# Optimization experiments

Hardware: AMD Instinct MI355X
Metric: run time of the kernel (lower is better)

## Reference

```python
import jax, jax.numpy as jnp
import numpy as np

B, C, T, H, W = 2, 128, 4, 32, 32
L = 6  # number_of_layers


def setup_inputs() -> dict:
    key = jax.random.key(0)
    ks = jax.random.split(key, 7)
    scale = 0.05  # keep pre-softmax logits in a sane range
    return {
        "x": jax.random.normal(ks[0], (B, C, T, H, W), dtype=jnp.float32),
        "W1": jax.random.normal(ks[1], (L, C, C), dtype=jnp.float32) * scale,
        "b1": jax.random.normal(ks[2], (L, C), dtype=jnp.float32) * scale,
        "W2": jax.random.normal(ks[3], (L, C, C), dtype=jnp.float32) * scale,
        "b2": jax.random.normal(ks[4], (L, C), dtype=jnp.float32) * scale,
        "Wg": jax.random.normal(ks[5], (L, C, C), dtype=jnp.float32) * scale,
        "bg": jax.random.normal(ks[6], (L, C), dtype=jnp.float32) * scale,
    }


def reference(x, W1, b1, W2, b2, Wg, bg):
    b, c, t, h, w = x.shape
    n = t * h * w  # THW tokens
    xf = x.reshape(b, c, n)  # [B, C, N], token order = (t, h, w) flattened
    inv_sqrt = 1.0 / jnp.sqrt(jnp.asarray(n, x.dtype))
    num_layers = W1.shape[0]
    acc = jnp.zeros((b, n, c), dtype=x.dtype)
    for l in range(num_layers):
        # conv3d 1x1x1 == per-token channel matmul + bias
        f1 = jnp.einsum('oc,bcn->bno', W1[l], xf) + b1[l]            # queries [B, N, C]
        f2 = jnp.einsum('oc,bcn->bon', W2[l], xf) + b2[l][:, None]   # keys    [B, C, N]
        scores = jnp.einsum('bnc,bcm->bnm', f1, f2) * inv_sqrt       # [B, N, N]
        # NOTE: original uses nn.Softmax(dim=1) -> normalize over the ROW (query) axis
        attn = jax.nn.softmax(scores, axis=1)
        g1 = jnp.einsum('oc,bcn->bno', Wg[l], xf) + bg[l]            # values [B, N, C]
        acc = acc + jnp.einsum('bnm,bmc->bnc', attn, g1)
    out = acc / num_layers                                           # mean over heads
    out = out.transpose(0, 2, 1).reshape(b, c, t, h, w)
    return out + x                                                    # residual
```

## Files before the change

kernel.cpp:

```cpp
#include <hip/hip_runtime.h>
#include <hip/hip_bf16.h>

#define BCNT 2
#define CCH  128
#define NTOK 4096
#define NLAY 6
#define QK8SCALE 0.15014030f

using f32x4   = __attribute__((ext_vector_type(4))) float;
using f32x16  = __attribute__((ext_vector_type(16))) float;
using bf16x8  = __attribute__((ext_vector_type(8))) short;

static __device__ __forceinline__ ushort f2bf(float f) {
  unsigned u = __float_as_uint(f);
  u += 0x7FFF + ((u >> 16) & 1);
  return (ushort)(u >> 16);
}
static __device__ __forceinline__ uint pk2(float lo, float hi) {
  uint r;
  asm volatile("v_cvt_pk_bf16_f32 %0, %1, %2" : "=v"(r) : "v"(lo), "v"(hi));
  return r;
}
static __device__ __forceinline__ uint pkf8(float a, float b) {
  uint r = 0;
  asm volatile("v_cvt_pk_fp8_f32 %0, %1, %2" : "+v"(r) : "v"(a), "v"(b));
  return r;
}
static __device__ __forceinline__ void plswap(uint& a, uint& b) {
  asm volatile("v_permlane32_swap_b32 %0, %1" : "+v"(a), "+v"(b));
}
static __device__ __forceinline__ float vexp2(float x) {
  float r;
  asm("v_exp_f32 %0, %1" : "=v"(r) : "v"(x));
  return r;
}
static __device__ __forceinline__ void dma16(const void* g, void* l) {
  __builtin_amdgcn_global_load_lds(
      (const __attribute__((address_space(1))) unsigned int*)g,
      (__attribute__((address_space(3))) unsigned int*)l, 16, 0, 0);
}

__global__ __launch_bounds__(256) void transpose_kernel(
    const float* __restrict__ x, ushort* __restrict__ xT)
{
  __shared__ ushort ls[64][68];
  const int t = threadIdx.x;
  const int ntile = blockIdx.x * 64, ctile = blockIdx.y * 64, b = blockIdx.z;
  const float* xb = x + ((size_t)b * CCH + ctile) * NTOK + ntile;
  #pragma unroll
  for (int p = 0; p < 4; ++p) {
    int idx = p * 256 + t;
    int cc = idx >> 4, n4 = (idx & 15) * 4;
    float4 v = *(const float4*)(xb + (size_t)cc * NTOK + n4);
    ls[cc][n4 + 0] = f2bf(v.x); ls[cc][n4 + 1] = f2bf(v.y);
    ls[cc][n4 + 2] = f2bf(v.z); ls[cc][n4 + 3] = f2bf(v.w);
  }
  __syncthreads();
  ushort* ob = xT + ((size_t)b * NTOK + ntile) * CCH + ctile;
  #pragma unroll
  for (int p = 0; p < 16; ++p) {
    int idx = p * 256 + t;
    int nn = idx >> 6, cc = idx & 63;
    ob[(size_t)nn * CCH + cc] = ls[cc][nn];
  }
}

__global__ __launch_bounds__(256) void wcvt_kernel(
    const float* __restrict__ W1, const float* __restrict__ W2,
    const float* __restrict__ Wg, ushort* __restrict__ Wb)
{
  const float* src = (blockIdx.y == 0) ? W1 : (blockIdx.y == 1) ? W2 : Wg;
  const size_t base = (size_t)blockIdx.y * NLAY * CCH * CCH;
  const size_t i = (size_t)blockIdx.x * 1024 + threadIdx.x * 4;
  float4 w = *(const float4*)(src + i);
  uint2 o = make_uint2(pk2(w.x, w.y), pk2(w.z, w.w));
  *(uint2*)(Wb + base + i) = o;
}

__global__ __launch_bounds__(256) void qkv_kernel(
    const ushort* __restrict__ xT, const ushort* __restrict__ Wb,
    const float* __restrict__ b1, const float* __restrict__ b2,
    const float* __restrict__ bg,
    uchar* __restrict__ q8, uchar* __restrict__ k8, ushort* __restrict__ vv,
    int l0)
{
  __shared__ __align__(16) ushort as[128][128];
  __shared__ __align__(16) ushort bs[128][128];
  const int t = threadIdx.x;
  const int lane = t & 63, wave = t >> 6;
  const int ntile = blockIdx.x * 128;
  const int which = blockIdx.y;
  const int z = blockIdx.z;
  const int b = z & 1, lidx = z >> 1, layer = l0 + lidx;
  const float* bias = (which == 0 ? b1 : which == 1 ? b2 : bg)
                      + (size_t)layer * CCH;
  const ushort* W = Wb + ((size_t)which * NLAY + layer) * CCH * CCH;
  const ushort* xb = xT + ((size_t)b * NTOK + ntile) * CCH;
  const ushort* ga = (which < 2) ? xb : W;
  const ushort* gb = (which < 2) ? W : xb;

  #pragma unroll
  for (int j = 0; j < 8; ++j) {
    int row = wave * 32 + j * 4 + (lane >> 4);
    int qs = (lane & 15) ^ (row & 15);
    dma16(ga + (size_t)row * 128 + qs * 8, &as[wave * 32 + j * 4][0]);
    dma16(gb + (size_t)row * 128 + qs * 8, &bs[wave * 32 + j * 4][0]);
  }
  asm volatile("s_waitcnt vmcnt(0)" ::: "memory");
  __syncthreads();

  const int l16 = lane & 15, lg = lane >> 4;
  const int wr = (wave >> 1) * 64, wc = (wave & 1) * 64;

  f32x4 acc[4][4];
  #pragma unroll
  for (int i = 0; i < 4; ++i)
    #pragma unroll
    for (int j = 0; j < 4; ++j) acc[i][j] = (f32x4)0.f;

  #pragma unroll
  for (int kk = 0; kk < 4; ++kk) {
    bf16x8 a[4], bb[4];
    #pragma unroll
    for (int i = 0; i < 4; ++i) {
      int row = wr + i * 16 + l16;
      a[i] = *(const bf16x8*)&as[row][(((kk * 4 + lg) ^ (row & 15)) * 8)];
    }
    #pragma unroll
    for (int j = 0; j < 4; ++j) {
      int row = wc + j * 16 + l16;
      bb[j] = *(const bf16x8*)&bs[row][(((kk * 4 + lg) ^ (row & 15)) * 8)];
    }
    #pragma unroll
    for (int i = 0; i < 4; ++i)
      #pragma unroll
      for (int j = 0; j < 4; ++j)
        acc[i][j] = __builtin_amdgcn_mfma_f32_16x16x32_bf16(a[i], bb[j], acc[i][j], 0, 0, 0);
  }

  if (which < 2) {
    uchar* o8 = (which == 0 ? q8 : k8) + (size_t)z * NTOK * CCH;
    #pragma unroll
    for (int j = 0; j < 4; ++j) {
      float bv = bias[wc + j * 16 + l16];
      #pragma unroll
      for (int i = 0; i < 4; ++i)
        #pragma unroll
        for (int r = 0; r < 4; ++r) {
          int n = ntile + wr + i * 16 + lg * 4 + r;
          float val = (acc[i][j][r] + bv) * QK8SCALE;
          uint pb = pkf8(val, val);
          o8[(size_t)n * CCH + wc + j * 16 + l16] = (uchar)pb;
        }
    }
  } else {
    ushort* oz = vv + (size_t)z * NTOK * CCH;
    #pragma unroll
    for (int i = 0; i < 4; ++i)
      #pragma unroll
      for (int r = 0; r < 4; ++r) {
        int o = wr + i * 16 + lg * 4 + r;
        float bv = bias[o];
        #pragma unroll
        for (int j = 0; j < 4; ++j)
          oz[(size_t)o * NTOK + ntile + wc + j * 16 + l16] = f2bf(acc[i][j][r] + bv);
      }
  }
}

__global__ __launch_bounds__(256, 3) void dsum_kernel(
    const uchar* __restrict__ q8, const uchar* __restrict__ k8,
    float* __restrict__ D)
{
  __shared__ __align__(16) uchar ks[3][32][256];
  const int t = threadIdx.x;
  const int lane = t & 63, wave = t >> 6;
  const int l31 = lane & 31, hi = lane >> 5;

  const int bid = blockIdx.x, ngrid = gridDim.x;
  const int wg = (bid & 7) * (ngrid >> 3) + (bid >> 3);
  const int z = wg >> 6, rem = wg & 63;
  const int nbase = (rem >> 3) * 512 + wave * 128;
  const int mstart = (rem & 7) * 512;

  const uchar* qz = q8 + (size_t)z * NTOK * CCH;
  const uchar* kz = k8 + (size_t)z * NTOK * CCH;

  long qf[4][8];
  #pragma unroll
  for (int nb = 0; nb < 4; ++nb)
    #pragma unroll
    for (int ck = 0; ck < 8; ++ck)
      qf[nb][ck] = *(const long*)(qz + (size_t)(nbase + nb * 32 + l31) * CCH
                                  + ck * 16 + hi * 8);

#define STAGEK(p, msub) do {                                                  \
    _Pragma("unroll")                                                         \
    for (int d_ = 0; d_ < 2; ++d_) {                                          \
      int R_ = wave * 8 + d_ * 4 + (lane >> 4);                               \
      int qs_ = (lane & 15) ^ (R_ & 15);                                      \
      dma16(kz + (size_t)((msub) + 2 * R_ + (qs_ >> 3)) * CCH + (qs_ & 7) * 16, \
            &ks[p][wave * 8 + d_ * 4][0]);                                    \
    }                                                                         \
  } while (0)

  STAGEK(0, mstart);
  STAGEK(1, mstart + 64);
  asm volatile("s_waitcnt vmcnt(2)" ::: "memory");
  __builtin_amdgcn_s_barrier();

  float* Dz = D + (size_t)z * NTOK;
  #pragma unroll
  for (int st = 0; st < 8; ++st) {
    if (st + 2 < 8) STAGEK((st + 2) % 3, mstart + (st + 2) * 64);
    const int cur = st % 3;

    #pragma unroll
    for (int mbi = 0; mbi < 2; ++mbi) {
      const int mb = mbi ^ (wave & 1);
      f32x16 ss[4];
      #pragma unroll
      for (int nb = 0; nb < 4; ++nb) ss[nb] = (f32x16)0.f;
      const int row = mb * 32 + l31;
      const int R = row >> 1;
      __builtin_amdgcn_s_setprio(1);
      #pragma unroll
      for (int ck = 0; ck < 8; ++ck) {
        int qs = ((row & 1) << 3) | ck;
        long kf = *(const long*)&ks[cur][R][((qs ^ (R & 15)) << 4) + hi * 8];
        #pragma unroll
        for (int nb = 0; nb < 4; ++nb)
          ss[nb] = __builtin_amdgcn_mfma_f32_32x32x16_fp8_fp8(qf[nb][ck], kf, ss[nb], 0, 0, 0);
      }
      __builtin_amdgcn_s_setprio(0);
      float s = 0.f;
      #pragma unroll
      for (int nb = 0; nb < 4; ++nb)
        #pragma unroll
        for (int r = 0; r < 16; ++r) s += vexp2(ss[nb][r]);
      s += __shfl_xor(s, 32);
      if (lane < 32)
        atomicAdd(&Dz[mstart + st * 64 + mb * 32 + l31], s);
    }
    if (st < 7) {
      asm volatile("s_waitcnt vmcnt(4)" ::: "memory");
      __builtin_amdgcn_s_barrier();
    }
  }
#undef STAGEK
}

__global__ __launch_bounds__(256) void scalev_kernel(
    ushort* __restrict__ vv, const float* __restrict__ D)
{
  size_t i8 = ((size_t)blockIdx.x * 256 + threadIdx.x) * 8;
  int m = (int)(i8 & (NTOK - 1));
  int z = (int)(i8 >> 19);
  const float* dp = D + (size_t)z * NTOK + m;
  uint4 u = *(uint4*)(vv + i8);
  float4 d0 = *(const float4*)dp;
  float4 d1 = *(const float4*)(dp + 4);
  uint w[4] = {u.x, u.y, u.z, u.w};
  float ds[8] = {d0.x, d0.y, d0.z, d0.w, d1.x, d1.y, d1.z, d1.w};
  #pragma unroll
  for (int d = 0; d < 4; ++d) {
    float r0 = __builtin_amdgcn_rcpf(ds[2 * d] * (float)NLAY);
    float r1 = __builtin_amdgcn_rcpf(ds[2 * d + 1] * (float)NLAY);
    float lo = __uint_as_float(w[d] << 16) * r0;
    float hi = __uint_as_float(w[d] & 0xFFFF0000u) * r1;
    w[d] = pk2(lo, hi);
  }
  *(uint4*)(vv + i8) = make_uint4(w[0], w[1], w[2], w[3]);
}

template <int NL, bool PART>
__global__ __launch_bounds__(256, 2) void pv_kernel(
    const uchar* __restrict__ q8, const uchar* __restrict__ k8,
    const ushort* __restrict__ vv, float* __restrict__ accG,
    ushort* __restrict__ part)
{
  __shared__ __align__(16) uchar  ks[3][32][256];
  __shared__ __align__(16) ushort vs[3][64][128];
  const int t = threadIdx.x;
  const int lane = t & 63, wave = t >> 6;
  const int l31 = lane & 31, hi = lane >> 5;
  const size_t PLZ = (size_t)NTOK * CCH;

  const int bid = blockIdx.x, ngrid = gridDim.x;
  const int wg = (bid & 7) * (ngrid >> 3) + (bid >> 3);
  const int b = wg >> 8, rem = wg & 255;
  const int ng = rem & 15, ms = rem >> 4;
  const int nbase = ng * 256 + wave * 64;
  const int mstart = ms * 256;

  long qf[2][8];
  f32x16 oacc[2][4];
  #pragma unroll
  for (int nb = 0; nb < 2; ++nb)
    #pragma unroll
    for (int cb = 0; cb < 4; ++cb) oacc[nb][cb] = (f32x16)0.f;

#define LOADQ(lidx) do {                                                      \
    const uchar* qz_ = q8 + (size_t)((lidx) * 2 + b) * PLZ;                   \
    _Pragma("unroll")                                                         \
    for (int nb_ = 0; nb_ < 2; ++nb_)                                         \
      _Pragma("unroll")                                                       \
      for (int ck_ = 0; ck_ < 8; ++ck_)                                       \
        qf[nb_][ck_] = *(const long*)(qz_ + (size_t)(nbase + nb_ * 32 + l31) * CCH \
                                      + ck_ * 16 + hi * 8);                   \
  } while (0)

#define STAGE(p, tau) do {                                                    \
    const uchar*  kz_ = k8 + (size_t)(((tau) >> 2) * 2 + b) * PLZ;            \
    const ushort* vz_ = vv + (size_t)(((tau) >> 2) * 2 + b) * PLZ;            \
    const int msub_ = mstart + ((tau) & 3) * 64;                              \
    _Pragma("unroll")                                                         \
    for (int d_ = 0; d_ < 2; ++d_) {                                          \
      int R_ = wave * 8 + d_ * 4 + (lane >> 4);                               \
      int qs_ = (lane & 15) ^ (R_ & 15);                                      \
      dma16(kz_ + (size_t)(msub_ + 2 * R_ + (qs_ >> 3)) * CCH + (qs_ & 7) * 16, \
            &ks[p][wave * 8 + d_ * 4][0]);                                    \
    }                                                                         \
    _Pragma("unroll")                                                         \
    for (int d_ = 0; d_ < 4; ++d_) {                                          \
      int r_ = wave * 16 + d_ * 4 + (lane >> 4);                              \
      int qs_ = (lane & 15) ^ (r_ & 15);                                      \
      dma16(vz_ + (size_t)(r_ + 64 * (qs_ >> 3)) * NTOK + msub_ + (qs_ & 7) * 8, \
            &vs[p][wave * 16 + d_ * 4][0]);                                   \
    }                                                                         \
  } while (0)

  STAGE(0, 0);
  STAGE(1, 1);

  #pragma unroll 3
  for (int tau = 0; tau < 4 * NL; ++tau) {
    asm volatile("s_waitcnt vmcnt(6)" ::: "memory");
    __builtin_amdgcn_s_barrier();
    if ((tau & 3) == 0) LOADQ(tau >> 2);
    if (tau + 2 < 4 * NL) STAGE((tau + 2) % 3, tau + 2);
    const int cur = tau % 3;

    #pragma unroll
    for (int mbi = 0; mbi < 2; ++mbi) {
      const int mb = mbi ^ (wave & 1);
      f32x16 ss[2];
      ss[0] = (f32x16)0.f; ss[1] = (f32x16)0.f;
      const int row = mb * 32 + l31;
      const int R = row >> 1;
      __builtin_amdgcn_s_setprio(1);
      #pragma unroll
      for (int ck = 0; ck < 8; ++ck) {
        int qs = ((row & 1) << 3) | ck;
        long kf = *(const long*)&ks[cur][R][((qs ^ (R & 15)) << 4) + hi * 8];
        ss[0] = __builtin_amdgcn_mfma_f32_32x32x16_fp8_fp8(kf, qf[0][ck], ss[0], 0, 0, 0);
        ss[1] = __builtin_amdgcn_mfma_f32_32x32x16_fp8_fp8(kf, qf[1][ck], ss[1], 0, 0, 0);
      }
      __builtin_amdgcn_s_setprio(0);

      bf16x8 paL[2][2];
      #pragma unroll
      for (int nb = 0; nb < 2; ++nb) {
        #pragma unroll
        for (int s = 0; s < 2; ++s) {
          uint w0 = pk2(vexp2(ss[nb][8 * s + 0]), vexp2(ss[nb][8 * s + 1]));
          uint w1 = pk2(vexp2(ss[nb][8 * s + 2]), vexp2(ss[nb][8 * s + 3]));
          uint w2 = pk2(vexp2(ss[nb][8 * s + 4]), vexp2(ss[nb][8 * s + 5]));
          uint w3 = pk2(vexp2(ss[nb][8 * s + 6]), vexp2(ss[nb][8 * s + 7]));
          plswap(w0, w2);
          plswap(w1, w3);
          uint4 ui = make_uint4(w0, w1, w2, w3);
          paL[nb][s] = *(bf16x8*)&ui;
        }
      }

      __builtin_amdgcn_s_setprio(1);
      #pragma unroll
      for (int cb = 0; cb < 4; ++cb) {
        const int c = cb * 32 + l31;
        const int r = c & 63;
        #pragma unroll
        for (int s = 0; s < 2; ++s) {
          int qs = ((c >> 6) << 3) | (4 * mb + 2 * s + hi);
          bf16x8 vf = *(const bf16x8*)&vs[cur][r][(qs ^ (r & 15)) * 8];
          oacc[0][cb] = __builtin_amdgcn_mfma_f32_32x32x16_bf16(paL[0][s], vf, oacc[0][cb], 0, 0, 0);
          oacc[1][cb] = __builtin_amdgcn_mfma_f32_32x32x16_bf16(paL[1][s], vf, oacc[1][cb], 0, 0, 0);
        }
      }
      __builtin_amdgcn_s_setprio(0);
    }
  }
#undef STAGE
#undef LOADQ

  if (PART) {
    ushort* pz = part + (size_t)(ms * BCNT + b) * NTOK * CCH;
    #pragma unroll
    for (int nb = 0; nb < 2; ++nb)
      #pragma unroll
      for (int cb = 0; cb < 4; ++cb)
        #pragma unroll
        for (int r = 0; r < 16; ++r) {
          int n = nbase + nb * 32 + (r & 3) + 8 * (r >> 2) + 4 * hi;
          pz[(size_t)n * CCH + cb * 32 + l31] = f2bf(oacc[nb][cb][r]);
        }
  } else {
    float* az = accG + (size_t)b * NTOK * CCH;
    #pragma unroll
    for (int nb = 0; nb < 2; ++nb)
      #pragma unroll
      for (int cb = 0; cb < 4; ++cb)
        #pragma unroll
        for (int r = 0; r < 16; ++r) {
          int n = nbase + nb * 32 + (r & 3) + 8 * (r >> 2) + 4 * hi;
          atomicAdd(&az[(size_t)n * CCH + cb * 32 + l31], oacc[nb][cb][r]);
        }
  }
}

__global__ __launch_bounds__(256) void finalize_kernel(
    const float* __restrict__ acc, const float* __restrict__ x,
    float* __restrict__ out)
{
  __shared__ float ts[64][65];
  const int t = threadIdx.x;
  const int ntile = blockIdx.x * 64, ctile = blockIdx.y * 64, b = blockIdx.z;
  const float* ab = acc + ((size_t)b * NTOK + ntile) * CCH + ctile;
  #pragma unroll
  for (int p = 0; p < 4; ++p) {
    int idx = p * 256 + t;
    int nn = idx >> 4, c4 = (idx & 15) * 4;
    float4 v = *(const float4*)(ab + (size_t)nn * CCH + c4);
    ts[nn][c4 + 0] = v.x; ts[nn][c4 + 1] = v.y;
    ts[nn][c4 + 2] = v.z; ts[nn][c4 + 3] = v.w;
  }
  __syncthreads();
  const size_t base = ((size_t)b * CCH + ctile) * NTOK + ntile;
  #pragma unroll
  for (int p = 0; p < 16; ++p) {
    int idx = p * 256 + t;
    int nn = idx & 63, cc = idx >> 6;
    size_t o = base + (size_t)cc * NTOK + nn;
    out[o] = ts[nn][cc] + x[o];
  }
}

__global__ __launch_bounds__(256) void finalize_part_kernel(
    const ushort* __restrict__ part, const float* __restrict__ x,
    float* __restrict__ out)
{
  __shared__ float ts[64][65];
  const int t = threadIdx.x;
  const int ntile = blockIdx.x * 64, ctile = blockIdx.y * 64, b = blockIdx.z;
  #pragma unroll
  for (int p = 0; p < 4; ++p) {
    int idx = p * 256 + t;
    int nn = idx >> 4, c4 = (idx & 15) * 4;
    float s0 = 0.f, s1 = 0.f, s2 = 0.f, s3 = 0.f;
    const ushort* pp = part + ((size_t)b * NTOK + ntile + nn) * CCH + ctile + c4;
    #pragma unroll
    for (int msi = 0; msi < 16; ++msi) {
      uint2 u = *(const uint2*)(pp + (size_t)msi * BCNT * NTOK * CCH);
      s0 += __uint_as_float(u.x << 16);
      s1 += __uint_as_float(u.x & 0xFFFF0000u);
      s2 += __uint_as_float(u.y << 16);
      s3 += __uint_as_float(u.y & 0xFFFF0000u);
    }
    ts[nn][c4 + 0] = s0; ts[nn][c4 + 1] = s1;
    ts[nn][c4 + 2] = s2; ts[nn][c4 + 3] = s3;
  }
  __syncthreads();
  const size_t base = ((size_t)b * CCH + ctile) * NTOK + ntile;
  #pragma unroll
  for (int p = 0; p < 16; ++p) {
    int idx = p * 256 + t;
    int nn = idx & 63, cc = idx >> 6;
    size_t o = base + (size_t)cc * NTOK + nn;
    out[o] = ts[nn][cc] + x[o];
  }
}

extern "C" void kernel_launch(void* const* d_in, const int* in_sizes, int n_in,
                              void* d_out, int out_size, void* d_ws, size_t ws_size,
                              hipStream_t stream)
{
  const float* x  = (const float*)d_in[0];
  const float* W1 = (const float*)d_in[1];
  const float* b1 = (const float*)d_in[2];
  const float* W2 = (const float*)d_in[3];
  const float* b2 = (const float*)d_in[4];
  const float* Wg = (const float*)d_in[5];
  const float* bg = (const float*)d_in[6];
  float* out = (float*)d_out;

  const size_t PL = (size_t)BCNT * NTOK * CCH;
  const size_t DSZ = (size_t)BCNT * NTOK;
  const size_t WBSZ = (size_t)3 * NLAY * CCH * CCH;

  int nb = 1;
  for (int cand : {6, 3, 2}) {
    size_t need = PL * 2 + (size_t)cand * (PL * 2 + PL + PL) + WBSZ * 2
                + (size_t)cand * DSZ * 4 + PL * 4;
    if (ws_size >= need) { nb = cand; break; }
  }
  size_t need_base = PL * 2 + (size_t)nb * (PL * 2 + PL + PL) + WBSZ * 2
                   + (size_t)nb * DSZ * 4 + PL * 4;
  bool usePart = (nb == 6) && (ws_size >= need_base + 16 * PL * 2);

  char* p = (char*)d_ws;
  ushort* xT = (ushort*)p; p += PL * 2;
  ushort* vv = (ushort*)p; p += (size_t)nb * PL * 2;
  uchar*  q8 = (uchar*)p;  p += (size_t)nb * PL;
  uchar*  k8 = (uchar*)p;  p += (size_t)nb * PL;
  ushort* Wb = (ushort*)p; p += WBSZ * 2;
  float*  D  = (float*)p;  p += (size_t)nb * DSZ * 4;
  float*  acc= (float*)p;  p += PL * 4;
  ushort* part = (ushort*)p;

  if (!usePart) hipMemsetAsync(acc, 0, PL * 4, stream);
  transpose_kernel<<<dim3(NTOK / 64, CCH / 64, BCNT), 256, 0, stream>>>(x, xT);
  wcvt_kernel<<<dim3(96, 3), 256, 0, stream>>>(W1, W2, Wg, Wb);

  for (int l0 = 0; l0 < NLAY; l0 += nb) {
    const int LB = nb * BCNT;
    hipMemsetAsync(D, 0, (size_t)LB * NTOK * 4, stream);
    qkv_kernel<<<dim3(NTOK / 128, 3, LB), 256, 0, stream>>>(
        xT, Wb, b1, b2, bg, q8, k8, vv, l0);
    dsum_kernel<<<dim3(LB * 64), 256, 0, stream>>>(q8, k8, D);
    scalev_kernel<<<dim3(LB * 256), 256, 0, stream>>>(vv, D);
    const dim3 pvg(BCNT * 256);
    if (usePart) {
      pv_kernel<6, true><<<pvg, 256, 0, stream>>>(q8, k8, vv, acc, part);
    } else {
      switch (nb) {
        case 6: pv_kernel<6, false><<<pvg, 256, 0, stream>>>(q8, k8, vv, acc, part); break;
        case 3: pv_kernel<3, false><<<pvg, 256, 0, stream>>>(q8, k8, vv, acc, part); break;
        case 2: pv_kernel<2, false><<<pvg, 256, 0, stream>>>(q8, k8, vv, acc, part); break;
        default: pv_kernel<1, false><<<pvg, 256, 0, stream>>>(q8, k8, vv, acc, part); break;
      }
    }
  }
  if (usePart)
    finalize_part_kernel<<<dim3(NTOK / 64, CCH / 64, BCNT), 256, 0, stream>>>(part, x, out);
  else
    finalize_kernel<<<dim3(NTOK / 64, CCH / 64, BCNT), 256, 0, stream>>>(acc, x, out);
}
```

Measured before the change: 168.4 us.

## Use FP8 PV matmul and 32x32x64 scaled MFMA for QK and PV

Switches the QK score matmuls in dsum and pv kernels from 32x32x16 fp8 MFMA to the wider 32x32x64 f8f6f4 scaled MFMA, loading 32-byte fragments. Converts the normalized V to fp8, with a pre-scale of 4096 to keep values in fp8 range, and the softmax probabilities to fp8, so the PV product also runs on fp8 MFMA; the output is descaled at accumulation. This halves the V bytes staged through LDS and the MFMA count, at the cost of lower precision in P and V and an extra fp8 V buffer in the workspace.

Result: slower. 235.0 us (+39.5%).

```diff
diff --git a/kernel.cpp b/kernel.cpp
--- a/kernel.cpp
+++ b/kernel.cpp
@@ -6,10 +6,12 @@
 #define NTOK 4096
 #define NLAY 6
 #define QK8SCALE 0.15014030f
+#define VDESC 2.44140625e-4f
 
 using f32x4   = __attribute__((ext_vector_type(4))) float;
 using f32x16  = __attribute__((ext_vector_type(16))) float;
 using bf16x8  = __attribute__((ext_vector_type(8))) short;
+using i32x8   = __attribute__((ext_vector_type(8))) int;
 
 static __device__ __forceinline__ ushort f2bf(float f) {
   unsigned u = __float_as_uint(f);
@@ -21,6 +23,12 @@
   asm volatile("v_cvt_pk_bf16_f32 %0, %1, %2" : "=v"(r) : "v"(lo), "v"(hi));
   return r;
 }
+static __device__ __forceinline__ uint pkf8x4(float a, float b, float c, float d) {
+  uint r;
+  asm volatile("v_cvt_pk_fp8_f32 %0, %1, %2" : "=v"(r) : "v"(a), "v"(b));
+  asm volatile("v_cvt_pk_fp8_f32 %0, %1, %2 op_sel:[0,0,1]" : "+v"(r) : "v"(c), "v"(d));
+  return r;
+}
 static __device__ __forceinline__ uint pkf8(float a, float b) {
   uint r = 0;
   asm volatile("v_cvt_pk_fp8_f32 %0, %1, %2" : "+v"(r) : "v"(a), "v"(b));
@@ -38,6 +46,15 @@
   __builtin_amdgcn_global_load_lds(
       (const __attribute__((address_space(1))) unsigned int*)g,
       (__attribute__((address_space(3))) unsigned int*)l, 16, 0, 0);
+}
+static __device__ __forceinline__ i32x8 cat8(uint4 a, uint4 b) {
+  i32x8 r;
+  r[0] = (int)a.x; r[1] = (int)a.y; r[2] = (int)a.z; r[3] = (int)a.w;
+  r[4] = (int)b.x; r[5] = (int)b.y; r[6] = (int)b.z; r[7] = (int)b.w;
+  return r;
+}
+static __device__ __forceinline__ f32x16 mxm(i32x8 a, i32x8 b, f32x16 c) {
+  return __builtin_amdgcn_mfma_scale_f32_32x32x64_f8f6f4(a, b, c, 0, 0, 0, 127, 0, 127);
 }
 
 __global__ __launch_bounds__(256) void transpose_kernel(
@@ -186,13 +203,13 @@
   const uchar* qz = q8 + (size_t)z * NTOK * CCH;
   const uchar* kz = k8 + (size_t)z * NTOK * CCH;
 
-  long qf[4][8];
+  i32x8 qf[4][2];
   #pragma unroll
   for (int nb = 0; nb < 4; ++nb)
     #pragma unroll
-    for (int ck = 0; ck < 8; ++ck)
-      qf[nb][ck] = *(const long*)(qz + (size_t)(nbase + nb * 32 + l31) * CCH
-                                  + ck * 16 + hi * 8);
+    for (int kk = 0; kk < 2; ++kk)
+      qf[nb][kk] = *(const i32x8*)(qz + (size_t)(nbase + nb * 32 + l31) * CCH
+                                   + kk * 64 + hi * 32);
 
 #define STAGEK(p, msub) do {                                                  \
     _Pragma("unroll")                                                         \
@@ -225,12 +242,14 @@
       const int R = row >> 1;
       __builtin_amdgcn_s_setprio(1);
       #pragma unroll
-      for (int ck = 0; ck < 8; ++ck) {
-        int qs = ((row & 1) << 3) | ck;
-        long kf = *(const long*)&ks[cur][R][((qs ^ (R & 15)) << 4) + hi * 8];
+      for (int kk = 0; kk < 2; ++kk) {
+        int p0 = (((row & 1) << 3) | (kk * 4 + hi * 2)) ^ (R & 15);
+        uint4 ka = *(const uint4*)&ks[cur][R][p0 * 16];
+        uint4 kb = *(const uint4*)&ks[cur][R][(p0 ^ 1) * 16];
+        i32x8 kf = cat8(ka, kb);
         #pragma unroll
         for (int nb = 0; nb < 4; ++nb)
-          ss[nb] = __builtin_amdgcn_mfma_f32_32x32x16_fp8_fp8(qf[nb][ck], kf, ss[nb], 0, 0, 0);
+          ss[nb] = mxm(qf[nb][kk], kf, ss[nb]);
       }
       __builtin_amdgcn_s_setprio(0);
       float s = 0.f;
@@ -251,36 +270,39 @@
 }
 
 __global__ __launch_bounds__(256) void scalev_kernel(
-    ushort* __restrict__ vv, const float* __restrict__ D)
+    const ushort* __restrict__ vv, const float* __restrict__ D,
+    uchar* __restrict__ v8)
 {
   size_t i8 = ((size_t)blockIdx.x * 256 + threadIdx.x) * 8;
   int m = (int)(i8 & (NTOK - 1));
   int z = (int)(i8 >> 19);
   const float* dp = D + (size_t)z * NTOK + m;
-  uint4 u = *(uint4*)(vv + i8);
+  uint4 u = *(const uint4*)(vv + i8);
   float4 d0 = *(const float4*)dp;
   float4 d1 = *(const float4*)(dp + 4);
   uint w[4] = {u.x, u.y, u.z, u.w};
   float ds[8] = {d0.x, d0.y, d0.z, d0.w, d1.x, d1.y, d1.z, d1.w};
+  float x[8];
   #pragma unroll
   for (int d = 0; d < 4; ++d) {
-    float r0 = __builtin_amdgcn_rcpf(ds[2 * d] * (float)NLAY);
-    float r1 = __builtin_amdgcn_rcpf(ds[2 * d + 1] * (float)NLAY);
-    float lo = __uint_as_float(w[d] << 16) * r0;
-    float hi = __uint_as_float(w[d] & 0xFFFF0000u) * r1;
-    w[d] = pk2(lo, hi);
-  }
-  *(uint4*)(vv + i8) = make_uint4(w[0], w[1], w[2], w[3]);
+    float r0 = __builtin_amdgcn_rcpf(ds[2 * d] * (NLAY / 4096.0f));
+    float r1 = __builtin_amdgcn_rcpf(ds[2 * d + 1] * (NLAY / 4096.0f));
+    x[2 * d]     = __uint_as_float(w[d] << 16) * r0;
+    x[2 * d + 1] = __uint_as_float(w[d] & 0xFFFF0000u) * r1;
+  }
+  uint2 o = make_uint2(pkf8x4(x[0], x[1], x[2], x[3]),
+                       pkf8x4(x[4], x[5], x[6], x[7]));
+  *(uint2*)(v8 + i8) = o;
 }
 
 template <int NL, bool PART>
 __global__ __launch_bounds__(256, 2) void pv_kernel(
     const uchar* __restrict__ q8, const uchar* __restrict__ k8,
-    const ushort* __restrict__ vv, float* __restrict__ accG,
+    const uchar* __restrict__ v8, float* __restrict__ accG,
     ushort* __restrict__ part)
 {
-  __shared__ __align__(16) uchar  ks[3][32][256];
-  __shared__ __align__(16) ushort vs[3][64][128];
+  __shared__ __align__(16) uchar ks[3][32][256];
+  __shared__ __align__(16) uchar vs[3][32][256];
   const int t = threadIdx.x;
   const int lane = t & 63, wave = t >> 6;
   const int l31 = lane & 31, hi = lane >> 5;
@@ -293,7 +315,7 @@
   const int nbase = ng * 256 + wave * 64;
   const int mstart = ms * 256;
 
-  long qf[2][8];
+  i32x8 qf[2][2];
   f32x16 oacc[2][4];
   #pragma unroll
   for (int nb = 0; nb < 2; ++nb)
@@ -305,14 +327,14 @@
     _Pragma("unroll")                                                         \
     for (int nb_ = 0; nb_ < 2; ++nb_)                                         \
       _Pragma("unroll")                                                       \
-      for (int ck_ = 0; ck_ < 8; ++ck_)                                       \
-        qf[nb_][ck_] = *(const long*)(qz_ + (size_t)(nbase + nb_ * 32 + l31) * CCH \
-                                      + ck_ * 16 + hi * 8);                   \
+      for (int kk_ = 0; kk_ < 2; ++kk_)                                       \
+        qf[nb_][kk_] = *(const i32x8*)(qz_ + (size_t)(nbase + nb_ * 32 + l31) * CCH \
+                                       + kk_ * 64 + hi * 32);                 \
   } while (0)
 
 #define STAGE(p, tau) do {                                                    \
-    const uchar*  kz_ = k8 + (size_t)(((tau) >> 2) * 2 + b) * PLZ;            \
-    const ushort* vz_ = vv + (size_t)(((tau) >> 2) * 2 + b) * PLZ;            \
+    const uchar* kz_ = k8 + (size_t)(((tau) >> 2) * 2 + b) * PLZ;             \
+    const uchar* vz_ = v8 + (size_t)(((tau) >> 2) * 2 + b) * PLZ;             \
     const int msub_ = mstart + ((tau) & 3) * 64;                              \
     _Pragma("unroll")                                                         \
     for (int d_ = 0; d_ < 2; ++d_) {                                          \
@@ -320,13 +342,9 @@
       int qs_ = (lane & 15) ^ (R_ & 15);                                      \
       dma16(kz_ + (size_t)(msub_ + 2 * R_ + (qs_ >> 3)) * CCH + (qs_ & 7) * 16, \
             &ks[p][wave * 8 + d_ * 4][0]);                                    \
-    }                                                                         \
-    _Pragma("unroll")                                                         \
-    for (int d_ = 0; d_ < 4; ++d_) {                                          \
-      int r_ = wave * 16 + d_ * 4 + (lane >> 4);                              \
-      int qs_ = (lane & 15) ^ (r_ & 15);                                      \
-      dma16(vz_ + (size_t)(r_ + 64 * (qs_ >> 3)) * NTOK + msub_ + (qs_ & 7) * 8, \
-            &vs[p][wave * 16 + d_ * 4][0]);                                   \
+      int c_ = R_ * 4 + (qs_ >> 2);                                           \
+      dma16(vz_ + (size_t)c_ * NTOK + msub_ + (qs_ & 3) * 16,                 \
+            &vs[p][wave * 8 + d_ * 4][0]);                                    \
     }                                                                         \
   } while (0)
 
@@ -335,60 +353,65 @@
 
   #pragma unroll 3
   for (int tau = 0; tau < 4 * NL; ++tau) {
-    asm volatile("s_waitcnt vmcnt(6)" ::: "memory");
+    asm volatile("s_waitcnt vmcnt(4)" ::: "memory");
     __builtin_amdgcn_s_barrier();
     if ((tau & 3) == 0) LOADQ(tau >> 2);
     if (tau + 2 < 4 * NL) STAGE((tau + 2) % 3, tau + 2);
     const int cur = tau % 3;
 
-    #pragma unroll
-    for (int mbi = 0; mbi < 2; ++mbi) {
-      const int mb = mbi ^ (wave & 1);
-      f32x16 ss[2];
-      ss[0] = (f32x16)0.f; ss[1] = (f32x16)0.f;
+    uint Uw[2][4], Vw[2][4];
+    #pragma unroll
+    for (int mb = 0; mb < 2; ++mb) {
+      f32x16 ss0 = (f32x16)0.f, ss1 = (f32x16)0.f;
       const int row = mb * 32 + l31;
       const int R = row >> 1;
       __builtin_amdgcn_s_setprio(1);
       #pragma unroll
-      for (int ck = 0; ck < 8; ++ck) {
-        int qs = ((row & 1) << 3) | ck;
-        long kf = *(const long*)&ks[cur][R][((qs ^ (R & 15)) << 4) + hi * 8];
-        ss[0] = __builtin_amdgcn_mfma_f32_32x32x16_fp8_fp8(kf, qf[0][ck], ss[0], 0, 0, 0);
-        ss[1] = __builtin_amdgcn_mfma_f32_32x32x16_fp8_fp8(kf, qf[1][ck], ss[1], 0, 0, 0);
+      for (int kk = 0; kk < 2; ++kk) {
+        int p0 = (((row & 1) << 3) | (kk * 4 + hi * 2)) ^ (R & 15);
+        uint4 ka = *(const uint4*)&ks[cur][R][p0 * 16];
+        uint4 kb = *(const uint4*)&ks[cur][R][(p0 ^ 1) * 16];
+        i32x8 kf = cat8(ka, kb);
+        ss0 = mxm(kf, qf[0][kk], ss0);
+        ss1 = mxm(kf, qf[1][kk], ss1);
       }
       __builtin_amdgcn_s_setprio(0);
-
-      bf16x8 paL[2][2];
-      #pragma unroll
-      for (int nb = 0; nb < 2; ++nb) {
-        #pragma unroll
-        for (int s = 0; s < 2; ++s) {
-          uint w0 = pk2(vexp2(ss[nb][8 * s + 0]), vexp2(ss[nb][8 * s + 1]));
-          uint w1 = pk2(vexp2(ss[nb][8 * s + 2]), vexp2(ss[nb][8 * s + 3]));
-          uint w2 = pk2(vexp2(ss[nb][8 * s + 4]), vexp2(ss[nb][8 * s + 5]));
-          uint w3 = pk2(vexp2(ss[nb][8 * s + 6]), vexp2(ss[nb][8 * s + 7]));
-          plswap(w0, w2);
-          plswap(w1, w3);
-          uint4 ui = make_uint4(w0, w1, w2, w3);
-          paL[nb][s] = *(bf16x8*)&ui;
-        }
+      #pragma unroll
+      for (int j = 0; j < 4; ++j) {
+        uint w0 = pkf8x4(vexp2(ss0[4 * j]), vexp2(ss0[4 * j + 1]),
+                         vexp2(ss0[4 * j + 2]), vexp2(ss0[4 * j + 3]));
+        uint w1 = pkf8x4(vexp2(ss1[4 * j]), vexp2(ss1[4 * j + 1]),
+                         vexp2(ss1[4 * j + 2]), vexp2(ss1[4 * j + 3]));
+        if (mb == 0) { Uw[0][j] = w0; Uw[1][j] = w1; }
+        else         { Vw[0][j] = w0; Vw[1][j] = w1; }
       }
-
-      __builtin_amdgcn_s_setprio(1);
-      #pragma unroll
-      for (int cb = 0; cb < 4; ++cb) {
-        const int c = cb * 32 + l31;
-        const int r = c & 63;
-        #pragma unroll
-        for (int s = 0; s < 2; ++s) {
-          int qs = ((c >> 6) << 3) | (4 * mb + 2 * s + hi);
-          bf16x8 vf = *(const bf16x8*)&vs[cur][r][(qs ^ (r & 15)) * 8];
-          oacc[0][cb] = __builtin_amdgcn_mfma_f32_32x32x16_bf16(paL[0][s], vf, oacc[0][cb], 0, 0, 0);
-          oacc[1][cb] = __builtin_amdgcn_mfma_f32_32x32x16_bf16(paL[1][s], vf, oacc[1][cb], 0, 0, 0);
-        }
-      }
-      __builtin_amdgcn_s_setprio(0);
-    }
+    }
+
+    i32x8 pa[2];
+    #pragma unroll
+    for (int nb = 0; nb < 2; ++nb) {
+      uint u0 = Uw[nb][0], u1 = Uw[nb][1], u2 = Uw[nb][2], u3 = Uw[nb][3];
+      uint v0 = Vw[nb][0], v1 = Vw[nb][1], v2 = Vw[nb][2], v3 = Vw[nb][3];
+      plswap(u0, v0); plswap(u1, v1); plswap(u2, v2); plswap(u3, v3);
+      i32x8 f;
+      f[0] = (int)u0; f[1] = (int)v0; f[2] = (int)u1; f[3] = (int)v1;
+      f[4] = (int)u2; f[5] = (int)v2; f[6] = (int)u3; f[7] = (int)v3;
+      pa[nb] = f;
+    }
+
+    __builtin_amdgcn_s_setprio(1);
+    #pragma unroll
+    for (int cb = 0; cb < 4; ++cb) {
+      const int c = cb * 32 + l31;
+      const int R2 = c >> 2;
+      int p0 = (((c & 3) << 2) | (hi << 1)) ^ (R2 & 15);
+      uint4 va = *(const uint4*)&vs[cur][R2][p0 * 16];
+      uint4 vb = *(const uint4*)&vs[cur][R2][(p0 ^ 1) * 16];
+      i32x8 vf = cat8(va, vb);
+      oacc[0][cb] = mxm(pa[0], vf, oacc[0][cb]);
+      oacc[1][cb] = mxm(pa[1], vf, oacc[1][cb]);
+    }
+    __builtin_amdgcn_s_setprio(0);
   }
 #undef STAGE
 #undef LOADQ
@@ -402,7 +425,7 @@
         #pragma unroll
         for (int r = 0; r < 16; ++r) {
           int n = nbase + nb * 32 + (r & 3) + 8 * (r >> 2) + 4 * hi;
-          pz[(size_t)n * CCH + cb * 32 + l31] = f2bf(oacc[nb][cb][r]);
+          pz[(size_t)n * CCH + cb * 32 + l31] = f2bf(oacc[nb][cb][r] * VDESC);
         }
   } else {
     float* az = accG + (size_t)b * NTOK * CCH;
@@ -413,7 +436,7 @@
         #pragma unroll
         for (int r = 0; r < 16; ++r) {
           int n = nbase + nb * 32 + (r & 3) + 8 * (r >> 2) + 4 * hi;
-          atomicAdd(&az[(size_t)n * CCH + cb * 32 + l31], oacc[nb][cb][r]);
+          atomicAdd(&az[(size_t)n * CCH + cb * 32 + l31], oacc[nb][cb][r] * VDESC);
         }
   }
 }
@@ -499,11 +522,11 @@
 
   int nb = 1;
   for (int cand : {6, 3, 2}) {
-    size_t need = PL * 2 + (size_t)cand * (PL * 2 + PL + PL) + WBSZ * 2
+    size_t need = PL * 2 + (size_t)cand * (PL * 2 + PL + PL + PL) + WBSZ * 2
                 + (size_t)cand * DSZ * 4 + PL * 4;
     if (ws_size >= need) { nb = cand; break; }
   }
-  size_t need_base = PL * 2 + (size_t)nb * (PL * 2 + PL + PL) + WBSZ * 2
+  size_t need_base = PL * 2 + (size_t)nb * (PL * 2 + PL + PL + PL) + WBSZ * 2
                    + (size_t)nb * DSZ * 4 + PL * 4;
   bool usePart = (nb == 6) && (ws_size >= need_base + 16 * PL * 2);
 
@@ -512,6 +535,7 @@
   ushort* vv = (ushort*)p; p += (size_t)nb * PL * 2;
   uchar*  q8 = (uchar*)p;  p += (size_t)nb * PL;
   uchar*  k8 = (uchar*)p;  p += (size_t)nb * PL;
+  uchar*  v8 = (uchar*)p;  p += (size_t)nb * PL;
   ushort* Wb = (ushort*)p; p += WBSZ * 2;
   float*  D  = (float*)p;  p += (size_t)nb * DSZ * 4;
   float*  acc= (float*)p;  p += PL * 4;
@@ -527,16 +551,16 @@
     qkv_kernel<<<dim3(NTOK / 128, 3, LB), 256, 0, stream>>>(
         xT, Wb, b1, b2, bg, q8, k8, vv, l0);
     dsum_kernel<<<dim3(LB * 64), 256, 0, stream>>>(q8, k8, D);
-    scalev_kernel<<<dim3(LB * 256), 256, 0, stream>>>(vv, D);
+    scalev_kernel<<<dim3(LB * 256), 256, 0, stream>>>(vv, D, v8);
     const dim3 pvg(BCNT * 256);
     if (usePart) {
-      pv_kernel<6, true><<<pvg, 256, 0, stream>>>(q8, k8, vv, acc, part);
+      pv_kernel<6, true><<<pvg, 256, 0, stream>>>(q8, k8, v8, acc, part);
     } else {
       switch (nb) {
-        case 6: pv_kernel<6, false><<<pvg, 256, 0, stream>>>(q8, k8, vv, acc, part); break;
-        case 3: pv_kernel<3, false><<<pvg, 256, 0, stream>>>(q8, k8, vv, acc, part); break;
-        case 2: pv_kernel<2, false><<<pvg, 256, 0, stream>>>(q8, k8, vv, acc, part); break;
-        default: pv_kernel<1, false><<<pvg, 256, 0, stream>>>(q8, k8, vv, acc, part); break;
+        case 6: pv_kernel<6, false><<<pvg, 256, 0, stream>>>(q8, k8, v8, acc, part); break;
+        case 3: pv_kernel<3, false><<<pvg, 256, 0, stream>>>(q8, k8, v8, acc, part); break;
+        case 2: pv_kernel<2, false><<<pvg, 256, 0, stream>>>(q8, k8, v8, acc, part); break;
+        default: pv_kernel<1, false><<<pvg, 256, 0, stream>>>(q8, k8, v8, acc, part); break;
       }
     }
   }
```
